# Performance work log

Measured on AMD Instinct MI355X. Metric: run time of the kernel, lower is better.

Reference implementation:

```python
import jax, jax.numpy as jnp
import numpy as np

PRECISION_RATIO = 0.1
ROUTE_THRESH = 0.05

def ternary_quantize(W):
    # TWN-style: delta = 0.7*mean|W|, alpha = mean of kept magnitudes
    delta = 0.7 * jnp.mean(jnp.abs(W))
    mask = (jnp.abs(W) > delta).astype(W.dtype)
    alpha = jnp.sum(jnp.abs(W) * mask) / jnp.maximum(jnp.sum(mask), 1.0)
    return alpha * jnp.sign(W) * mask

def rpb_weight(W, precision_ratio=PRECISION_RATIO):
    # Ternary base + full-precision residual kept for top `precision_ratio` of entries
    Wq = ternary_quantize(W)
    res = W - Wq
    k = max(1, int(precision_ratio * W.size))
    kth = jax.lax.top_k(jnp.abs(res).reshape(-1), k)[0][-1]
    keep = (jnp.abs(res) >= kth).astype(W.dtype)
    return Wq + res * keep

def selective_route(x, threshold=ROUTE_THRESH):
    return x * (jnp.abs(x) >= threshold).astype(x.dtype)

def _lin(x, W, b):
    return x @ W.T + b

def setup_inputs() -> dict:
    key = jax.random.key(0)
    ks = jax.random.split(key, 24)
    B = 8192
    dims = {"vision": 2048, "text": 1024, "audio": 512}
    D = 1024
    T = D * 3  # total_dim = 3072
    s = 0.02
    inp = {
        "x_vision": jax.random.normal(ks[0], (B, dims["vision"]), jnp.float32),
        "x_text": jax.random.normal(ks[1], (B, dims["text"]), jnp.float32),
        "x_audio": jax.random.normal(ks[2], (B, dims["audio"]), jnp.float32),
        "Wv": jax.random.normal(ks[3], (D, dims["vision"]), jnp.float32) * s,
        "bv": jnp.zeros((D,), jnp.float32),
        "Wt": jax.random.normal(ks[4], (D, dims["text"]), jnp.float32) * s,
        "bt": jnp.zeros((D,), jnp.float32),
        "Wa": jax.random.normal(ks[5], (D, dims["audio"]), jnp.float32) * s,
        "ba": jnp.zeros((D,), jnp.float32),
        "Wq1": jax.random.normal(ks[6], (D, T), jnp.float32) * s,
        "bq1": jnp.zeros((D,), jnp.float32),
        "Wq2": jax.random.normal(ks[7], (D, D), jnp.float32) * s,
        "bq2": jnp.zeros((D,), jnp.float32),
        "Wf1": jax.random.normal(ks[8], (D, T), jnp.float32) * s,
        "bf1": jnp.zeros((D,), jnp.float32),
        "Wf2": jax.random.normal(ks[9], (D, D), jnp.float32) * s,
        "bf2": jnp.zeros((D,), jnp.float32),
        "mix_ratio": jnp.asarray(0.75, jnp.float32),
    }
    return inp

def reference(x_vision, x_text, x_audio, Wv, bv, Wt, bt, Wa, ba,
              Wq1, bq1, Wq2, bq2, Wf1, bf1, Wf2, bf2, mix_ratio):
    # per-modality projections then concat in modality order
    pv = _lin(x_vision, Wv, bv)
    pt = _lin(x_text, Wt, bt)
    pa = _lin(x_audio, Wa, ba)
    concat = jnp.concatenate([pv, pt, pa], axis=1)  # [B, 3*D]
    routed = selective_route(concat)
    # quantized (RPB) branch
    h = jax.nn.relu(_lin(routed, rpb_weight(Wq1), bq1))
    out_quant = _lin(h, rpb_weight(Wq2), bq2)
    # full-precision branch
    g = jax.nn.relu(_lin(concat, Wf1, bf1))
    out_full = _lin(g, Wf2, bf2)
    mix = jax.nn.sigmoid(mix_ratio)
    return mix * out_quant + (1.0 - mix) * out_full
```

## Files before the change

### kernel.cpp

```cpp
#include <hip/hip_runtime.h>


typedef _Float16 f16x8 __attribute__((ext_vector_type(8)));
typedef float f32x4 __attribute__((ext_vector_type(4)));

__device__ __forceinline__ unsigned short f16b(float v) {
  union { _Float16 h; unsigned short u; } cv; cv.h = (_Float16)v; return cv.u;
}

__device__ __forceinline__ void load_lds16(const void* g, void* l) {
  __builtin_amdgcn_global_load_lds(
      (const __attribute__((address_space(1))) void*)g,
      (__attribute__((address_space(3))) void*)l, 16, 0, 0);
}

__device__ __forceinline__ float sigmoidf_dev(float x) {
  return 1.0f / (1.0f + expf(-x));
}

__device__ __forceinline__ float reduce_region_f(const float* part, int lo, int hi,
                                                 float* sbuf) {
  float a = 0.f;
  for (int i = lo + threadIdx.x; i < hi; i += 256) a += part[i];
  sbuf[threadIdx.x] = a; __syncthreads();
  for (int o = 128; o > 0; o >>= 1) {
    if ((int)threadIdx.x < o) sbuf[threadIdx.x] += sbuf[threadIdx.x + o];
    __syncthreads();
  }
  float r = sbuf[0];
  __syncthreads();
  return r;
}

struct F2HArgs {
  const float* src[7];
  unsigned short* dst[7];
  long cum4[8];
};

__global__ void f2h_all(F2HArgs a) {
  long total = a.cum4[7];
  for (long i = (long)blockIdx.x * blockDim.x + threadIdx.x; i < total;
       i += (long)gridDim.x * blockDim.x) {
    int s = 0;
#pragma unroll
    for (int j = 1; j < 7; ++j) s += (i >= a.cum4[j]) ? 1 : 0;
    long off = i - a.cum4[s];
    float4 v = ((const float4*)a.src[s])[off];
    ushort4 o;
    o.x = f16b(v.x); o.y = f16b(v.y); o.z = f16b(v.z); o.w = f16b(v.w);
    ((ushort4*)a.dst[s])[off] = o;
  }
}

#define NB_W1 768
#define NB_TOT 1024

__global__ void part_abssum2(const float* __restrict__ W1, long n41,
                             const float* __restrict__ W2, long n42,
                             float* __restrict__ part, unsigned* __restrict__ hist) {
  __shared__ float s[256];
  if (blockIdx.x < 2) hist[blockIdx.x * 256 + threadIdx.x] = 0;
  int w = blockIdx.x < NB_W1 ? 0 : 1;
  const float4* W4 = (const float4*)(w ? W2 : W1);
  long n4 = w ? n42 : n41;
  int nb = w ? (NB_TOT - NB_W1) : NB_W1;
  int bid = w ? (int)blockIdx.x - NB_W1 : (int)blockIdx.x;
  float acc = 0.f;
  for (long i = (long)bid * blockDim.x + threadIdx.x; i < n4;
       i += (long)nb * blockDim.x) {
    float4 v = W4[i];
    acc += fabsf(v.x) + fabsf(v.y) + fabsf(v.z) + fabsf(v.w);
  }
  s[threadIdx.x] = acc; __syncthreads();
  for (int o = 128; o > 0; o >>= 1) {
    if ((int)threadIdx.x < o) s[threadIdx.x] += s[threadIdx.x + o];
    __syncthreads();
  }
  if (threadIdx.x == 0) part[blockIdx.x] = s[0];
}

__global__ void part_kept2(const float* __restrict__ W1, long S1,
                           const float* __restrict__ W2, long S2,
                           const float* __restrict__ part,
                           float* __restrict__ scal,
                           float* __restrict__ pb, unsigned* __restrict__ pc) {
  __shared__ float sf[256]; __shared__ unsigned sc[256];
  int w = blockIdx.x < NB_W1 ? 0 : 1;
  const float* W = w ? W2 : W1;
  long S = w ? S2 : S1;
  int nb = w ? (NB_TOT - NB_W1) : NB_W1;
  int bid = w ? (int)blockIdx.x - NB_W1 : (int)blockIdx.x;
  float tot = reduce_region_f(part, w ? NB_W1 : 0, w ? NB_TOT : NB_W1, sf);
  float delta = 0.7f * (tot / (float)S);
  if (bid == 0 && threadIdx.x == 0) scal[w * 2] = delta;
  float a = 0.f; unsigned c = 0;
  for (long i = (long)bid * blockDim.x + threadIdx.x; i < S;
       i += (long)nb * blockDim.x) {
    float aw = fabsf(W[i]);
    if (aw > delta) { a += aw; ++c; }
  }
  sf[threadIdx.x] = a; sc[threadIdx.x] = c; __syncthreads();
  for (int o = 128; o > 0; o >>= 1) {
    if ((int)threadIdx.x < o) { sf[threadIdx.x] += sf[threadIdx.x + o]; sc[threadIdx.x] += sc[threadIdx.x + o]; }
    __syncthreads();
  }
  if (threadIdx.x == 0) { pb[blockIdx.x] = sf[0]; pc[blockIdx.x] = sc[0]; }
}

__global__ void fin_alpha(const float* __restrict__ pb, const unsigned* __restrict__ pc,
                          float* __restrict__ scal) {
  __shared__ float sf[256]; __shared__ unsigned sc[256];
  int w = blockIdx.x;
  int lo = w ? NB_W1 : 0, hi = w ? NB_TOT : NB_W1;
  float a = 0.f; unsigned c = 0;
  for (int i = lo + threadIdx.x; i < hi; i += 256) { a += pb[i]; c += pc[i]; }
  sf[threadIdx.x] = a; sc[threadIdx.x] = c; __syncthreads();
  for (int o = 128; o > 0; o >>= 1) {
    if ((int)threadIdx.x < o) { sf[threadIdx.x] += sf[threadIdx.x + o]; sc[threadIdx.x] += sc[threadIdx.x + o]; }
    __syncthreads();
  }
  if (threadIdx.x == 0) {
    float cnt = (float)sc[0]; if (cnt < 1.f) cnt = 1.f;
    scal[w * 2 + 1] = sf[0] / cnt;
  }
}

__global__ void hist_pass2(const float* __restrict__ W1, long S1,
                           const float* __restrict__ W2, long S2,
                           const float* __restrict__ scal,
                           const unsigned* __restrict__ u,
                           unsigned* __restrict__ hist, int shift) {
  __shared__ unsigned h[256];
  h[threadIdx.x] = 0; __syncthreads();
  int w = blockIdx.x < NB_W1 ? 0 : 1;
  const float* W = w ? W2 : W1;
  long S = w ? S2 : S1;
  int nb = w ? (NB_TOT - NB_W1) : NB_W1;
  int bid = w ? (int)blockIdx.x - NB_W1 : (int)blockIdx.x;
  float delta = scal[w * 2], alpha = scal[w * 2 + 1];
  unsigned prefix = (shift >= 24) ? 0u : u[w * 4];
  int hs = shift + 8;
  for (long i = (long)bid * blockDim.x + threadIdx.x; i < S;
       i += (long)nb * blockDim.x) {
    float x = W[i];
    float aw = fabsf(x);
    float wq = (aw > delta) ? copysignf(alpha, x) : 0.0f;
    unsigned ub = __float_as_uint(fabsf(x - wq));
    bool ok = (hs >= 32) || ((ub >> hs) == (prefix >> hs));
    if (ok) atomicAdd(&h[(ub >> shift) & 255u], 1u);
  }
  __syncthreads();
  if (h[threadIdx.x]) atomicAdd(&hist[w * 256 + threadIdx.x], h[threadIdx.x]);
}

__global__ void sel_pass2(unsigned* __restrict__ hist, unsigned* __restrict__ u,
                          int shift, int first, int last,
                          unsigned k1, unsigned k2) {
  __shared__ unsigned h[256];
  int w = blockIdx.x, t = threadIdx.x;
  h[t] = hist[w * 256 + t];
  __syncthreads();
  if (t == 0) {
    unsigned krem = first ? (w ? k2 : k1) : u[w * 4 + 1];
    unsigned cum = 0, above = 0;
    int bstar = 0;
    for (int b = 255; b >= 0; --b) {
      unsigned nc = cum + h[b];
      if (nc >= krem) { bstar = b; above = cum; break; }
      cum = nc;
    }
    unsigned np = ((unsigned)bstar) << shift;
    u[w * 4 + 0] = first ? np : (u[w * 4 + 0] | np);
    u[w * 4 + 1] = krem - above;
    if (last) u[w * 4 + 2] = first ? np : u[w * 4 + 0];
  }
  __syncthreads();
  hist[w * 256 + t] = 0;
}

struct FinArgs {
  const float* Wq1; const float* Wq2; const float* Wf2;
  const float* bq2; const float* bf2; const float* mixp;
  const float* scal;
  const unsigned* u;
  unsigned short* wq1_h;
  unsigned short* w2_h;
  float* b2;
};

__global__ void finalize_weights(FinArgs a) {
  const long S1 = 3145728, S2 = 1048576, D = 1024;
  float mix = sigmoidf_dev(a.mixp[0]);
  long total = S1 + 2 * S2 + D;
  float d1 = a.scal[0], a1 = a.scal[1];
  float d2 = a.scal[2], a2 = a.scal[3];
  unsigned kth1 = a.u[2], kth2 = a.u[6];
  for (long i = (long)blockIdx.x * blockDim.x + threadIdx.x; i < total;
       i += (long)gridDim.x * blockDim.x) {
    if (i < S1) {
      float x = a.Wq1[i];
      float wq = (fabsf(x) > d1) ? copysignf(a1, x) : 0.0f;
      float res = x - wq;
      float v = wq + ((__float_as_uint(fabsf(res)) >= kth1) ? res : 0.0f);
      a.wq1_h[i] = f16b(v);
    } else if (i < S1 + S2) {
      long j = i - S1; int r = (int)(j >> 10), c = (int)(j & 1023);
      float x = a.Wq2[j];
      float wq = (fabsf(x) > d2) ? copysignf(a2, x) : 0.0f;
      float res = x - wq;
      float v = wq + ((__float_as_uint(fabsf(res)) >= kth2) ? res : 0.0f);
      a.w2_h[(long)r * 2048 + c] = f16b(mix * v);
    } else if (i < S1 + 2 * S2) {
      long j = i - S1 - S2; int r = (int)(j >> 10), c = (int)(j & 1023);
      a.w2_h[(long)r * 2048 + 1024 + c] = f16b((1.0f - mix) * a.Wf2[j]);
    } else {
      long j = i - S1 - 2 * S2;
      a.b2[j] = mix * a.bq2[j] + (1.0f - mix) * a.bf2[j];
    }
  }
}

struct GemmArgs {
  const unsigned short* A0; const unsigned short* A1; const unsigned short* A2;
  const unsigned short* B0; const unsigned short* B1; const unsigned short* B2;
  const float* c0; const float* c1; const float* c2;
  int K0, K1, K2;
  int nrows;
  int ldc;
  unsigned short* o0; unsigned short* o1; float* oF;
};

template <int EPI>
__global__ __launch_bounds__(512) void gemm6(GemmArgs g) {
  constexpr int AL = 128 * 32 * 2;
  constexpr int BL = 256 * 32 * 2;
  __shared__ __align__(16) char sm[2 * AL + 2 * BL];
  const int tid = threadIdx.x;
  const int wid = tid >> 6;
  const int lane = tid & 63;
  const int wm = wid >> 2, wn = wid & 3;

  const int nwg = gridDim.x;
  const int id = (blockIdx.x & 7) * (nwg >> 3) + (blockIdx.x >> 3);
  const int ncols = nwg / g.nrows;
  const int c = id % ncols, r = id / ncols;
  const int sel = c >> 2, lc = c & 3;

  const unsigned short* A = sel == 0 ? g.A0 : (sel == 1 ? g.A1 : g.A2);
  const unsigned short* Bw = sel == 0 ? g.B0 : (sel == 1 ? g.B1 : g.B2);
  const float* bias = sel == 0 ? g.c0 : (sel == 1 ? g.c1 : g.c2);
  const int K = sel == 0 ? g.K0 : (sel == 1 ? g.K1 : g.K2);
  const long brow = (long)r * 128;
  const int bRowB = lc * 256;

  f32x4 acc[4][4];
#pragma unroll
  for (int i = 0; i < 4; ++i)
#pragma unroll
    for (int j = 0; j < 4; ++j)
#pragma unroll
      for (int e = 0; e < 4; ++e) acc[i][j][e] = 0.f;

  const int oA = tid * 16;
  const unsigned short* aSrc = A + (brow + (oA >> 6)) * (long)K + ((oA & 63) >> 1);
  const unsigned short* bSrc[2];
#pragma unroll
  for (int j = 0; j < 2; ++j) {
    int o = j * 8192 + tid * 16;
    bSrc[j] = Bw + (long)(bRowB + (o >> 6)) * K + ((o & 63) >> 1);
  }

  auto STAGE = [&](int buf, int k0) {
    load_lds16(aSrc + k0, sm + (size_t)buf * AL + wid * 1024);
#pragma unroll
    for (int j = 0; j < 2; ++j)
      load_lds16(bSrc[j] + k0, sm + 2 * AL + (size_t)buf * BL + j * 8192 + wid * 1024);
  };

  const int kb = (lane >> 4) * 16;
  auto COMPUTE = [&](int buf) {
    const char* lAp = sm + (size_t)buf * AL;
    const char* lBp = sm + 2 * AL + (size_t)buf * BL;
    f16x8 a[4], b[4];
#pragma unroll
    for (int m = 0; m < 4; ++m)
      a[m] = *(const f16x8*)(lAp + (wm * 64 + m * 16 + (lane & 15)) * 64 + kb);
#pragma unroll
    for (int n = 0; n < 4; ++n)
      b[n] = *(const f16x8*)(lBp + (wn * 64 + n * 16 + (lane & 15)) * 64 + kb);
#pragma unroll
    for (int m = 0; m < 4; ++m)
#pragma unroll
      for (int n = 0; n < 4; ++n)
        acc[m][n] = __builtin_amdgcn_mfma_f32_16x16x32_f16(a[m], b[n], acc[m][n], 0, 0, 0);
  };

  const int NT = K >> 5;
  STAGE(0, 0);
  __syncthreads();
  int cur = 0;
  for (int t = 0; t < NT - 1; ++t) {
    STAGE(cur ^ 1, (t + 1) << 5);
    COMPUTE(cur);
    __syncthreads();
    cur ^= 1;
  }
  COMPUTE(cur);

  const int cb = c * 256 + wn * 64;
  const int rb = r * 128 + wm * 64;
  const int bcol0 = bRowB + wn * 64;
#pragma unroll
  for (int i = 0; i < 4; ++i) {
    int r0 = rb + i * 16 + ((lane >> 4) << 2);
#pragma unroll
    for (int j = 0; j < 4; ++j) {
      int ccol = cb + j * 16 + (lane & 15);
      float bb = bias[bcol0 + j * 16 + (lane & 15)];
#pragma unroll
      for (int e = 0; e < 4; ++e) {
        float v = acc[i][j][e] + bb;
        long idx = (long)(r0 + e) * g.ldc + ccol;
        if constexpr (EPI == 0) {
          g.o0[idx] = f16b(v);
          g.o1[idx] = f16b(fabsf(v) >= 0.05f ? v : 0.0f);
        } else if constexpr (EPI == 1) {
          g.o0[idx] = f16b(fmaxf(v, 0.0f));
        } else {
          g.oF[idx] = v;
        }
      }
    }
  }
}

extern "C" void kernel_launch(void* const* d_in, const int* in_sizes, int n_in,
                              void* d_out, int out_size, void* d_ws, size_t ws_size,
                              hipStream_t stream) {
  const float* xv = (const float*)d_in[0];
  const float* xt = (const float*)d_in[1];
  const float* xa = (const float*)d_in[2];
  const float* Wv = (const float*)d_in[3];
  const float* bv = (const float*)d_in[4];
  const float* Wt = (const float*)d_in[5];
  const float* bt = (const float*)d_in[6];
  const float* Wa = (const float*)d_in[7];
  const float* ba = (const float*)d_in[8];
  const float* Wq1 = (const float*)d_in[9];
  const float* bq1 = (const float*)d_in[10];
  const float* Wq2 = (const float*)d_in[11];
  const float* bq2 = (const float*)d_in[12];
  const float* Wf1 = (const float*)d_in[13];
  const float* bf1 = (const float*)d_in[14];
  const float* Wf2 = (const float*)d_in[15];
  const float* bf2 = (const float*)d_in[16];
  const float* mixp = (const float*)d_in[17];

  const int B = 8192, D = 1024, T = 3072;
  const int Kv = 2048, Kt = 1024, Ka = 512;
  const long S1 = (long)D * T, S2 = (long)D * D;

  char* w = (char*)d_ws;
  auto alloc = [&](size_t bytes) -> char* {
    char* p = w; w += (bytes + 255) & ~(size_t)255; return p;
  };
  unsigned short* xv_h = (unsigned short*)alloc((size_t)B * Kv * 2);
  unsigned short* xt_h = (unsigned short*)alloc((size_t)B * Kt * 2);
  unsigned short* xa_h = (unsigned short*)alloc((size_t)B * Ka * 2);
  unsigned short* wv_h = (unsigned short*)alloc((size_t)D * Kv * 2);
  unsigned short* wt_h = (unsigned short*)alloc((size_t)D * Kt * 2);
  unsigned short* wa_h = (unsigned short*)alloc((size_t)D * Ka * 2);
  unsigned short* wq1_h = (unsigned short*)alloc((size_t)D * T * 2);
  unsigned short* wf1_h = (unsigned short*)alloc((size_t)D * T * 2);
  unsigned short* w2_h = (unsigned short*)alloc((size_t)D * 2048 * 2);
  unsigned short* concat_h = (unsigned short*)alloc((size_t)B * T * 2);
  unsigned short* routed_h = (unsigned short*)alloc((size_t)B * T * 2);
  unsigned short* a2_h = (unsigned short*)alloc((size_t)B * 2048 * 2);
  float* b2 = (float*)alloc(D * 4);
  float* part = (float*)alloc(1024 * 4);
  float* pb = (float*)alloc(1024 * 4);
  unsigned* pc = (unsigned*)alloc(1024 * 4);
  float* scal = (float*)alloc(64);
  unsigned* u = (unsigned*)alloc(64);
  unsigned* hist = (unsigned*)alloc(2 * 256 * 4);

  F2HArgs fa;
  fa.src[0] = xv;  fa.dst[0] = xv_h;
  fa.src[1] = xt;  fa.dst[1] = xt_h;
  fa.src[2] = xa;  fa.dst[2] = xa_h;
  fa.src[3] = Wv;  fa.dst[3] = wv_h;
  fa.src[4] = Wt;  fa.dst[4] = wt_h;
  fa.src[5] = Wa;  fa.dst[5] = wa_h;
  fa.src[6] = Wf1; fa.dst[6] = wf1_h;
  long n4s[7] = {(long)B * Kv / 4, (long)B * Kt / 4, (long)B * Ka / 4,
                 (long)D * Kv / 4, (long)D * Kt / 4, (long)D * Ka / 4, S1 / 4};
  fa.cum4[0] = 0;
  for (int i = 0; i < 7; ++i) fa.cum4[i + 1] = fa.cum4[i] + n4s[i];
  f2h_all<<<2048, 256, 0, stream>>>(fa);

  part_abssum2<<<NB_TOT, 256, 0, stream>>>(Wq1, S1 / 4, Wq2, S2 / 4, part, hist);
  part_kept2<<<NB_TOT, 256, 0, stream>>>(Wq1, S1, Wq2, S2, part, scal, pb, pc);
  fin_alpha<<<2, 256, 0, stream>>>(pb, pc, scal);
  for (int rr = 0; rr < 4; ++rr) {
    hist_pass2<<<NB_TOT, 256, 0, stream>>>(Wq1, S1, Wq2, S2, scal, u, hist, 24 - 8 * rr);
    sel_pass2<<<2, 256, 0, stream>>>(hist, u, 24 - 8 * rr, rr == 0 ? 1 : 0,
                                     rr == 3 ? 1 : 0,
                                     (unsigned)(S1 / 10), (unsigned)(S2 / 10));
  }

  FinArgs fw;
  fw.Wq1 = Wq1; fw.Wq2 = Wq2; fw.Wf2 = Wf2;
  fw.bq2 = bq2; fw.bf2 = bf2; fw.mixp = mixp;
  fw.scal = scal; fw.u = u;
  fw.wq1_h = wq1_h; fw.w2_h = w2_h; fw.b2 = b2;
  finalize_weights<<<1024, 256, 0, stream>>>(fw);

  GemmArgs gp;
  gp.A0 = xv_h; gp.A1 = xt_h; gp.A2 = xa_h;
  gp.B0 = wv_h; gp.B1 = wt_h; gp.B2 = wa_h;
  gp.c0 = bv; gp.c1 = bt; gp.c2 = ba;
  gp.K0 = Kv; gp.K1 = Kt; gp.K2 = Ka;
  gp.nrows = B / 128; gp.ldc = T;
  gp.o0 = concat_h; gp.o1 = routed_h; gp.oF = nullptr;
  gemm6<0><<<12 * (B / 128), 512, 0, stream>>>(gp);

  GemmArgs gh;
  gh.A0 = routed_h; gh.A1 = concat_h; gh.A2 = routed_h;
  gh.B0 = wq1_h; gh.B1 = wf1_h; gh.B2 = wq1_h;
  gh.c0 = bq1; gh.c1 = bf1; gh.c2 = bq1;
  gh.K0 = T; gh.K1 = T; gh.K2 = T;
  gh.nrows = B / 128; gh.ldc = 2048;
  gh.o0 = a2_h; gh.o1 = nullptr; gh.oF = nullptr;
  gemm6<1><<<8 * (B / 128), 512, 0, stream>>>(gh);

  GemmArgs gf;
  gf.A0 = a2_h; gf.A1 = a2_h; gf.A2 = a2_h;
  gf.B0 = w2_h; gf.B1 = w2_h; gf.B2 = w2_h;
  gf.c0 = b2; gf.c1 = b2; gf.c2 = b2;
  gf.K0 = 2048; gf.K1 = 2048; gf.K2 = 2048;
  gf.nrows = B / 128; gf.ldc = D;
  gf.o0 = nullptr; gf.o1 = nullptr; gf.oF = (float*)d_out;
  gemm6<2><<<4 * (B / 128), 512, 0, stream>>>(gf);
}
```

Before: 424.3 us.

## Fuse preprocessing kernels, inline scalar reductions, and narrow final GEMM tile

Merges the fp16 conversion and the abs-sum partial reduction into one launch. It drops the fin_alpha kernel and the scal buffer by recomputing delta and alpha from partials inside each consumer block. It also templates the GEMM on the N tile width and runs the final K=2048 GEMM with 128-wide tiles, which doubles its grid to 512 blocks for better CU occupancy. In exchange, every block of hist_pass2 and finalize_weights now repeats small redundant reductions.

```diff
diff --git a/kernel.cpp b/kernel.cpp
--- a/kernel.cpp
+++ b/kernel.cpp
@@ -17,6 +17,9 @@
 __device__ __forceinline__ float sigmoidf_dev(float x) {
   return 1.0f / (1.0f + expf(-x));
 }
+
+#define NB_W1 768
+#define NB_TOT 1024
 
 __device__ __forceinline__ float reduce_region_f(const float* part, int lo, int hi,
                                                  float* sbuf) {
@@ -32,58 +35,72 @@
   return r;
 }
 
-struct F2HArgs {
+__device__ __forceinline__ float alpha_region(const float* pb, const unsigned* pc,
+                                              int lo, int hi, float* sf, unsigned* sc) {
+  float a = 0.f; unsigned c = 0;
+  for (int i = lo + threadIdx.x; i < hi; i += 256) { a += pb[i]; c += pc[i]; }
+  sf[threadIdx.x] = a; sc[threadIdx.x] = c; __syncthreads();
+  for (int o = 128; o > 0; o >>= 1) {
+    if ((int)threadIdx.x < o) { sf[threadIdx.x] += sf[threadIdx.x + o]; sc[threadIdx.x] += sc[threadIdx.x + o]; }
+    __syncthreads();
+  }
+  float s = sf[0]; float cnt = (float)sc[0];
+  __syncthreads();
+  if (cnt < 1.f) cnt = 1.f;
+  return s / cnt;
+}
+
+struct Pre1Args {
   const float* src[7];
   unsigned short* dst[7];
   long cum4[8];
+  const float* W1; long n41;
+  const float* W2; long n42;
+  float* part;
+  unsigned* hist;
 };
 
-__global__ void f2h_all(F2HArgs a) {
-  long total = a.cum4[7];
-  for (long i = (long)blockIdx.x * blockDim.x + threadIdx.x; i < total;
-       i += (long)gridDim.x * blockDim.x) {
-    int s = 0;
-#pragma unroll
-    for (int j = 1; j < 7; ++j) s += (i >= a.cum4[j]) ? 1 : 0;
-    long off = i - a.cum4[s];
-    float4 v = ((const float4*)a.src[s])[off];
-    ushort4 o;
-    o.x = f16b(v.x); o.y = f16b(v.y); o.z = f16b(v.z); o.w = f16b(v.w);
-    ((ushort4*)a.dst[s])[off] = o;
-  }
-}
-
-#define NB_W1 768
-#define NB_TOT 1024
-
-__global__ void part_abssum2(const float* __restrict__ W1, long n41,
-                             const float* __restrict__ W2, long n42,
-                             float* __restrict__ part, unsigned* __restrict__ hist) {
-  __shared__ float s[256];
-  if (blockIdx.x < 2) hist[blockIdx.x * 256 + threadIdx.x] = 0;
-  int w = blockIdx.x < NB_W1 ? 0 : 1;
-  const float4* W4 = (const float4*)(w ? W2 : W1);
-  long n4 = w ? n42 : n41;
-  int nb = w ? (NB_TOT - NB_W1) : NB_W1;
-  int bid = w ? (int)blockIdx.x - NB_W1 : (int)blockIdx.x;
-  float acc = 0.f;
-  for (long i = (long)bid * blockDim.x + threadIdx.x; i < n4;
-       i += (long)nb * blockDim.x) {
-    float4 v = W4[i];
-    acc += fabsf(v.x) + fabsf(v.y) + fabsf(v.z) + fabsf(v.w);
-  }
-  s[threadIdx.x] = acc; __syncthreads();
-  for (int o = 128; o > 0; o >>= 1) {
-    if ((int)threadIdx.x < o) s[threadIdx.x] += s[threadIdx.x + o];
-    __syncthreads();
-  }
-  if (threadIdx.x == 0) part[blockIdx.x] = s[0];
+__global__ void pre1(Pre1Args a) {
+  if (blockIdx.x < 2048) {
+    long total = a.cum4[7];
+    for (long i = (long)blockIdx.x * 256 + threadIdx.x; i < total;
+         i += (long)2048 * 256) {
+      int s = 0;
+#pragma unroll
+      for (int j = 1; j < 7; ++j) s += (i >= a.cum4[j]) ? 1 : 0;
+      long off = i - a.cum4[s];
+      float4 v = ((const float4*)a.src[s])[off];
+      ushort4 o;
+      o.x = f16b(v.x); o.y = f16b(v.y); o.z = f16b(v.z); o.w = f16b(v.w);
+      ((ushort4*)a.dst[s])[off] = o;
+    }
+  } else {
+    __shared__ float s[256];
+    int bid2 = (int)blockIdx.x - 2048;
+    if (bid2 < 2) a.hist[bid2 * 256 + threadIdx.x] = 0;
+    int w = bid2 < NB_W1 ? 0 : 1;
+    const float4* W4 = (const float4*)(w ? a.W2 : a.W1);
+    long n4 = w ? a.n42 : a.n41;
+    int nb = w ? (NB_TOT - NB_W1) : NB_W1;
+    int bid = w ? bid2 - NB_W1 : bid2;
+    float acc = 0.f;
+    for (long i = (long)bid * 256 + threadIdx.x; i < n4;
+         i += (long)nb * 256) {
+      float4 v = W4[i];
+      acc += fabsf(v.x) + fabsf(v.y) + fabsf(v.z) + fabsf(v.w);
+    }
+    s[threadIdx.x] = acc; __syncthreads();
+    for (int o = 128; o > 0; o >>= 1) {
+      if ((int)threadIdx.x < o) s[threadIdx.x] += s[threadIdx.x + o];
+      __syncthreads();
+    }
+    if (threadIdx.x == 0) a.part[bid2] = s[0];
+  }
 }
 
 __global__ void part_kept2(const float* __restrict__ W1, long S1,
                            const float* __restrict__ W2, long S2,
                            const float* __restrict__ part,
-                           float* __restrict__ scal,
                            float* __restrict__ pb, unsigned* __restrict__ pc) {
   __shared__ float sf[256]; __shared__ unsigned sc[256];
   int w = blockIdx.x < NB_W1 ? 0 : 1;
@@ -93,7 +110,6 @@
   int bid = w ? (int)blockIdx.x - NB_W1 : (int)blockIdx.x;
   float tot = reduce_region_f(part, w ? NB_W1 : 0, w ? NB_TOT : NB_W1, sf);
   float delta = 0.7f * (tot / (float)S);
-  if (bid == 0 && threadIdx.x == 0) scal[w * 2] = delta;
   float a = 0.f; unsigned c = 0;
   for (long i = (long)bid * blockDim.x + threadIdx.x; i < S;
        i += (long)nb * blockDim.x) {
@@ -108,37 +124,25 @@
   if (threadIdx.x == 0) { pb[blockIdx.x] = sf[0]; pc[blockIdx.x] = sc[0]; }
 }
 
-__global__ void fin_alpha(const float* __restrict__ pb, const unsigned* __restrict__ pc,
-                          float* __restrict__ scal) {
-  __shared__ float sf[256]; __shared__ unsigned sc[256];
-  int w = blockIdx.x;
-  int lo = w ? NB_W1 : 0, hi = w ? NB_TOT : NB_W1;
-  float a = 0.f; unsigned c = 0;
-  for (int i = lo + threadIdx.x; i < hi; i += 256) { a += pb[i]; c += pc[i]; }
-  sf[threadIdx.x] = a; sc[threadIdx.x] = c; __syncthreads();
-  for (int o = 128; o > 0; o >>= 1) {
-    if ((int)threadIdx.x < o) { sf[threadIdx.x] += sf[threadIdx.x + o]; sc[threadIdx.x] += sc[threadIdx.x + o]; }
-    __syncthreads();
-  }
-  if (threadIdx.x == 0) {
-    float cnt = (float)sc[0]; if (cnt < 1.f) cnt = 1.f;
-    scal[w * 2 + 1] = sf[0] / cnt;
-  }
-}
-
 __global__ void hist_pass2(const float* __restrict__ W1, long S1,
                            const float* __restrict__ W2, long S2,
-                           const float* __restrict__ scal,
+                           const float* __restrict__ part,
+                           const float* __restrict__ pb, const unsigned* __restrict__ pc,
                            const unsigned* __restrict__ u,
                            unsigned* __restrict__ hist, int shift) {
+  __shared__ float sf[256]; __shared__ unsigned sc[256];
   __shared__ unsigned h[256];
-  h[threadIdx.x] = 0; __syncthreads();
   int w = blockIdx.x < NB_W1 ? 0 : 1;
   const float* W = w ? W2 : W1;
   long S = w ? S2 : S1;
   int nb = w ? (NB_TOT - NB_W1) : NB_W1;
   int bid = w ? (int)blockIdx.x - NB_W1 : (int)blockIdx.x;
-  float delta = scal[w * 2], alpha = scal[w * 2 + 1];
+  int lo = w ? NB_W1 : 0, hi = w ? NB_TOT : NB_W1;
+  float tot = reduce_region_f(part, lo, hi, sf);
+  float delta = 0.7f * (tot / (float)S);
+  float alpha = alpha_region(pb, pc, lo, hi, sf, sc);
+  h[threadIdx.x] = 0;
+  __syncthreads();
   unsigned prefix = (shift >= 24) ? 0u : u[w * 4];
   int hs = shift + 8;
   for (long i = (long)bid * blockDim.x + threadIdx.x; i < S;
@@ -182,7 +186,7 @@
 struct FinArgs {
   const float* Wq1; const float* Wq2; const float* Wf2;
   const float* bq2; const float* bf2; const float* mixp;
-  const float* scal;
+  const float* part; const float* pb; const unsigned* pc;
   const unsigned* u;
   unsigned short* wq1_h;
   unsigned short* w2_h;
@@ -190,12 +194,17 @@
 };
 
 __global__ void finalize_weights(FinArgs a) {
+  __shared__ float sf[256]; __shared__ unsigned sc[256];
   const long S1 = 3145728, S2 = 1048576, D = 1024;
+  float tot1 = reduce_region_f(a.part, 0, NB_W1, sf);
+  float d1 = 0.7f * (tot1 / (float)S1);
+  float tot2 = reduce_region_f(a.part, NB_W1, NB_TOT, sf);
+  float d2 = 0.7f * (tot2 / (float)S2);
+  float a1 = alpha_region(a.pb, a.pc, 0, NB_W1, sf, sc);
+  float a2 = alpha_region(a.pb, a.pc, NB_W1, NB_TOT, sf, sc);
+  unsigned kth1 = a.u[2], kth2 = a.u[6];
   float mix = sigmoidf_dev(a.mixp[0]);
   long total = S1 + 2 * S2 + D;
-  float d1 = a.scal[0], a1 = a.scal[1];
-  float d2 = a.scal[2], a2 = a.scal[3];
-  unsigned kth1 = a.u[2], kth2 = a.u[6];
   for (long i = (long)blockIdx.x * blockDim.x + threadIdx.x; i < total;
        i += (long)gridDim.x * blockDim.x) {
     if (i < S1) {
@@ -228,13 +237,16 @@
   int K0, K1, K2;
   int nrows;
   int ldc;
+  int cpsl;
   unsigned short* o0; unsigned short* o1; float* oF;
 };
 
-template <int EPI>
-__global__ __launch_bounds__(512) void gemm6(GemmArgs g) {
+template <int EPI, int BN>
+__global__ __launch_bounds__(512) void gemm8(GemmArgs g) {
   constexpr int AL = 128 * 32 * 2;
-  constexpr int BL = 256 * 32 * 2;
+  constexpr int BL = BN * 32 * 2;
+  constexpr int BISS = BL / 8192;
+  constexpr int NR = BN / 4 / 16;
   __shared__ __align__(16) char sm[2 * AL + 2 * BL];
   const int tid = threadIdx.x;
   const int wid = tid >> 6;
@@ -245,28 +257,28 @@
   const int id = (blockIdx.x & 7) * (nwg >> 3) + (blockIdx.x >> 3);
   const int ncols = nwg / g.nrows;
   const int c = id % ncols, r = id / ncols;
-  const int sel = c >> 2, lc = c & 3;
+  const int sel = c >> g.cpsl, lc = c & ((1 << g.cpsl) - 1);
 
   const unsigned short* A = sel == 0 ? g.A0 : (sel == 1 ? g.A1 : g.A2);
   const unsigned short* Bw = sel == 0 ? g.B0 : (sel == 1 ? g.B1 : g.B2);
   const float* bias = sel == 0 ? g.c0 : (sel == 1 ? g.c1 : g.c2);
   const int K = sel == 0 ? g.K0 : (sel == 1 ? g.K1 : g.K2);
   const long brow = (long)r * 128;
-  const int bRowB = lc * 256;
-
-  f32x4 acc[4][4];
+  const int bRowB = lc * BN;
+
+  f32x4 acc[4][NR];
 #pragma unroll
   for (int i = 0; i < 4; ++i)
 #pragma unroll
-    for (int j = 0; j < 4; ++j)
+    for (int j = 0; j < NR; ++j)
 #pragma unroll
       for (int e = 0; e < 4; ++e) acc[i][j][e] = 0.f;
 
   const int oA = tid * 16;
   const unsigned short* aSrc = A + (brow + (oA >> 6)) * (long)K + ((oA & 63) >> 1);
-  const unsigned short* bSrc[2];
-#pragma unroll
-  for (int j = 0; j < 2; ++j) {
+  const unsigned short* bSrc[BISS];
+#pragma unroll
+  for (int j = 0; j < BISS; ++j) {
     int o = j * 8192 + tid * 16;
     bSrc[j] = Bw + (long)(bRowB + (o >> 6)) * K + ((o & 63) >> 1);
   }
@@ -274,7 +286,7 @@
   auto STAGE = [&](int buf, int k0) {
     load_lds16(aSrc + k0, sm + (size_t)buf * AL + wid * 1024);
 #pragma unroll
-    for (int j = 0; j < 2; ++j)
+    for (int j = 0; j < BISS; ++j)
       load_lds16(bSrc[j] + k0, sm + 2 * AL + (size_t)buf * BL + j * 8192 + wid * 1024);
   };
 
@@ -282,17 +294,17 @@
   auto COMPUTE = [&](int buf) {
     const char* lAp = sm + (size_t)buf * AL;
     const char* lBp = sm + 2 * AL + (size_t)buf * BL;
-    f16x8 a[4], b[4];
+    f16x8 a[4], b[NR];
 #pragma unroll
     for (int m = 0; m < 4; ++m)
       a[m] = *(const f16x8*)(lAp + (wm * 64 + m * 16 + (lane & 15)) * 64 + kb);
 #pragma unroll
-    for (int n = 0; n < 4; ++n)
-      b[n] = *(const f16x8*)(lBp + (wn * 64 + n * 16 + (lane & 15)) * 64 + kb);
+    for (int n = 0; n < NR; ++n)
+      b[n] = *(const f16x8*)(lBp + (wn * (BN / 4) + n * 16 + (lane & 15)) * 64 + kb);
 #pragma unroll
     for (int m = 0; m < 4; ++m)
 #pragma unroll
-      for (int n = 0; n < 4; ++n)
+      for (int n = 0; n < NR; ++n)
         acc[m][n] = __builtin_amdgcn_mfma_f32_16x16x32_f16(a[m], b[n], acc[m][n], 0, 0, 0);
   };
 
@@ -308,14 +320,14 @@
   }
   COMPUTE(cur);
 
-  const int cb = c * 256 + wn * 64;
+  const int cb = c * BN + wn * (BN / 4);
   const int rb = r * 128 + wm * 64;
-  const int bcol0 = bRowB + wn * 64;
+  const int bcol0 = bRowB + wn * (BN / 4);
 #pragma unroll
   for (int i = 0; i < 4; ++i) {
     int r0 = rb + i * 16 + ((lane >> 4) << 2);
 #pragma unroll
-    for (int j = 0; j < 4; ++j) {
+    for (int j = 0; j < NR; ++j) {
       int ccol = cb + j * 16 + (lane & 15);
       float bb = bias[bcol0 + j * 16 + (lane & 15)];
 #pragma unroll
@@ -381,38 +393,40 @@
   float* part = (float*)alloc(1024 * 4);
   float* pb = (float*)alloc(1024 * 4);
   unsigned* pc = (unsigned*)alloc(1024 * 4);
-  float* scal = (float*)alloc(64);
   unsigned* u = (unsigned*)alloc(64);
   unsigned* hist = (unsigned*)alloc(2 * 256 * 4);
 
-  F2HArgs fa;
-  fa.src[0] = xv;  fa.dst[0] = xv_h;
-  fa.src[1] = xt;  fa.dst[1] = xt_h;
-  fa.src[2] = xa;  fa.dst[2] = xa_h;
-  fa.src[3] = Wv;  fa.dst[3] = wv_h;
-  fa.src[4] = Wt;  fa.dst[4] = wt_h;
-  fa.src[5] = Wa;  fa.dst[5] = wa_h;
-  fa.src[6] = Wf1; fa.dst[6] = wf1_h;
+  const unsigned k1 = (unsigned)(S1 / 10), k2 = (unsigned)(S2 / 10);
+
+  Pre1Args pa;
+  pa.src[0] = xv;  pa.dst[0] = xv_h;
+  pa.src[1] = xt;  pa.dst[1] = xt_h;
+  pa.src[2] = xa;  pa.dst[2] = xa_h;
+  pa.src[3] = Wv;  pa.dst[3] = wv_h;
+  pa.src[4] = Wt;  pa.dst[4] = wt_h;
+  pa.src[5] = Wa;  pa.dst[5] = wa_h;
+  pa.src[6] = Wf1; pa.dst[6] = wf1_h;
   long n4s[7] = {(long)B * Kv / 4, (long)B * Kt / 4, (long)B * Ka / 4,
                  (long)D * Kv / 4, (long)D * Kt / 4, (long)D * Ka / 4, S1 / 4};
-  fa.cum4[0] = 0;
-  for (int i = 0; i < 7; ++i) fa.cum4[i + 1] = fa.cum4[i] + n4s[i];
-  f2h_all<<<2048, 256, 0, stream>>>(fa);
-
-  part_abssum2<<<NB_TOT, 256, 0, stream>>>(Wq1, S1 / 4, Wq2, S2 / 4, part, hist);
-  part_kept2<<<NB_TOT, 256, 0, stream>>>(Wq1, S1, Wq2, S2, part, scal, pb, pc);
-  fin_alpha<<<2, 256, 0, stream>>>(pb, pc, scal);
+  pa.cum4[0] = 0;
+  for (int i = 0; i < 7; ++i) pa.cum4[i + 1] = pa.cum4[i] + n4s[i];
+  pa.W1 = Wq1; pa.n41 = S1 / 4;
+  pa.W2 = Wq2; pa.n42 = S2 / 4;
+  pa.part = part; pa.hist = hist;
+  pre1<<<3072, 256, 0, stream>>>(pa);
+
+  part_kept2<<<NB_TOT, 256, 0, stream>>>(Wq1, S1, Wq2, S2, part, pb, pc);
   for (int rr = 0; rr < 4; ++rr) {
-    hist_pass2<<<NB_TOT, 256, 0, stream>>>(Wq1, S1, Wq2, S2, scal, u, hist, 24 - 8 * rr);
+    hist_pass2<<<NB_TOT, 256, 0, stream>>>(Wq1, S1, Wq2, S2, part, pb, pc,
+                                           u, hist, 24 - 8 * rr);
     sel_pass2<<<2, 256, 0, stream>>>(hist, u, 24 - 8 * rr, rr == 0 ? 1 : 0,
-                                     rr == 3 ? 1 : 0,
-                                     (unsigned)(S1 / 10), (unsigned)(S2 / 10));
+                                     rr == 3 ? 1 : 0, k1, k2);
   }
 
   FinArgs fw;
   fw.Wq1 = Wq1; fw.Wq2 = Wq2; fw.Wf2 = Wf2;
   fw.bq2 = bq2; fw.bf2 = bf2; fw.mixp = mixp;
-  fw.scal = scal; fw.u = u;
+  fw.part = part; fw.pb = pb; fw.pc = pc; fw.u = u;
   fw.wq1_h = wq1_h; fw.w2_h = w2_h; fw.b2 = b2;
   finalize_weights<<<1024, 256, 0, stream>>>(fw);
 
@@ -421,25 +435,25 @@
   gp.B0 = wv_h; gp.B1 = wt_h; gp.B2 = wa_h;
   gp.c0 = bv; gp.c1 = bt; gp.c2 = ba;
   gp.K0 = Kv; gp.K1 = Kt; gp.K2 = Ka;
-  gp.nrows = B / 128; gp.ldc = T;
+  gp.nrows = B / 128; gp.ldc = T; gp.cpsl = 2;
   gp.o0 = concat_h; gp.o1 = routed_h; gp.oF = nullptr;
-  gemm6<0><<<12 * (B / 128), 512, 0, stream>>>(gp);
+  gemm8<0, 256><<<12 * (B / 128), 512, 0, stream>>>(gp);
 
   GemmArgs gh;
   gh.A0 = routed_h; gh.A1 = concat_h; gh.A2 = routed_h;
   gh.B0 = wq1_h; gh.B1 = wf1_h; gh.B2 = wq1_h;
   gh.c0 = bq1; gh.c1 = bf1; gh.c2 = bq1;
   gh.K0 = T; gh.K1 = T; gh.K2 = T;
-  gh.nrows = B / 128; gh.ldc = 2048;
+  gh.nrows = B / 128; gh.ldc = 2048; gh.cpsl = 2;
   gh.o0 = a2_h; gh.o1 = nullptr; gh.oF = nullptr;
-  gemm6<1><<<8 * (B / 128), 512, 0, stream>>>(gh);
+  gemm8<1, 256><<<8 * (B / 128), 512, 0, stream>>>(gh);
 
   GemmArgs gf;
   gf.A0 = a2_h; gf.A1 = a2_h; gf.A2 = a2_h;
   gf.B0 = w2_h; gf.B1 = w2_h; gf.B2 = w2_h;
   gf.c0 = b2; gf.c1 = b2; gf.c2 = b2;
   gf.K0 = 2048; gf.K1 = 2048; gf.K2 = 2048;
-  gf.nrows = B / 128; gf.ldc = D;
+  gf.nrows = B / 128; gf.ldc = D; gf.cpsl = 3;
   gf.o0 = nullptr; gf.o1 = nullptr; gf.oF = (float*)d_out;
-  gemm6<2><<<4 * (B / 128), 512, 0, stream>>>(gf);
-}
+  gemm8<2, 128><<<8 * (B / 128), 512, 0, stream>>>(gf);
+}
```

New measurement: 421.7 us. No clear change (-0.6%).
